# Kernel tuning notes

Hardware: AMD Instinct MI355X
Metric: run time of the kernel (lower is better)

Reference implementation:

```python
import jax, jax.numpy as jnp
import numpy as np

TIMES = 16
SPIKE_THRESHOLD = 1.0
RESET_VALUE = 0.0


def setup_inputs() -> dict:
    key = jax.random.key(0)
    # dim 0 = TIMES * per-step batch (512); feature dim 8192
    inputs = jax.random.normal(key, (TIMES * 512, 8192), dtype=jnp.float32)
    return {"inputs": inputs}


def reference(inputs):
    # torch: inputs.split(shape[0] // times) -> TIMES chunks of [B, D]
    T = TIMES
    B = inputs.shape[0] // T
    xs = inputs.reshape(T, B, inputs.shape[1])  # [T, B, D]

    def step(V, I):
        V = V + I
        # V[V.abs() > thr] = reset_value
        V = jnp.where(jnp.abs(V) > SPIKE_THRESHOLD, jnp.float32(RESET_VALUE), V)
        return V, V

    V0 = jnp.zeros_like(xs[0])
    _, outs = jax.lax.scan(step, V0, xs)  # outs: [T, B, D]
    # torch.vstack(outputs) -> [T*B, D]
    return outs.reshape(inputs.shape)
```

## Files before the change

kernel.cpp:

```cpp
#include <hip/hip_runtime.h>


constexpr int TIMES = 16;
constexpr long long STEP_F4 = (512LL * 8192LL) / 4;

__global__ __launch_bounds__(256) void SpikeLayer_88553635709313_kernel(
    const float4* __restrict__ in, float4* __restrict__ out) {
    long long idx = (long long)blockIdx.x * blockDim.x + threadIdx.x;
    float4 V = make_float4(0.f, 0.f, 0.f, 0.f);
    long long p = idx;
#pragma unroll
    for (int t = 0; t < TIMES; ++t) {
        float4 I = in[p];
        V.x += I.x; V.y += I.y; V.z += I.z; V.w += I.w;
        V.x = (fabsf(V.x) > 1.0f) ? 0.0f : V.x;
        V.y = (fabsf(V.y) > 1.0f) ? 0.0f : V.y;
        V.z = (fabsf(V.z) > 1.0f) ? 0.0f : V.z;
        V.w = (fabsf(V.w) > 1.0f) ? 0.0f : V.w;
        out[p] = V;
        p += STEP_F4;
    }
}

extern "C" void kernel_launch(void* const* d_in, const int* in_sizes, int n_in,
                              void* d_out, int out_size, void* d_ws, size_t ws_size,
                              hipStream_t stream) {
    const float4* in = (const float4*)d_in[0];
    float4* out = (float4*)d_out;
    const int threads = 256;
    const int blocks = (int)(STEP_F4 / threads);
    SpikeLayer_88553635709313_kernel<<<blocks, threads, 0, stream>>>(in, out);
}
```

Baseline: 454.9 us.

## Process two columns per thread with software prefetch and nontemporal stores

Each thread now handles two float4 elements, one from each half of the per-step slab, which halves the grid. The next timestep's input is prefetched before the current step is computed, to raise memory-level parallelism. Outputs are written with nontemporal stores to reduce cache pollution. The risks are lower occupancy from halving the grid and extra register pressure.

```diff
diff --git a/kernel.cpp b/kernel.cpp
--- a/kernel.cpp
+++ b/kernel.cpp
@@ -1,33 +1,57 @@
 #include <hip/hip_runtime.h>
 
 
+typedef float f32x4 __attribute__((ext_vector_type(4)));
+
 constexpr int TIMES = 16;
 constexpr long long STEP_F4 = (512LL * 8192LL) / 4;
+constexpr long long HALF_F4 = STEP_F4 / 2;
+
+__device__ __forceinline__ f32x4 step_reset(f32x4 V, f32x4 I) {
+    V += I;
+    V.x = (fabsf(V.x) > 1.0f) ? 0.0f : V.x;
+    V.y = (fabsf(V.y) > 1.0f) ? 0.0f : V.y;
+    V.z = (fabsf(V.z) > 1.0f) ? 0.0f : V.z;
+    V.w = (fabsf(V.w) > 1.0f) ? 0.0f : V.w;
+    return V;
+}
 
 __global__ __launch_bounds__(256) void SpikeLayer_88553635709313_kernel(
-    const float4* __restrict__ in, float4* __restrict__ out) {
+    const f32x4* __restrict__ in, f32x4* __restrict__ out) {
     long long idx = (long long)blockIdx.x * blockDim.x + threadIdx.x;
-    float4 V = make_float4(0.f, 0.f, 0.f, 0.f);
-    long long p = idx;
+    long long pa = idx;
+    long long pb = idx + HALF_F4;
+
+    f32x4 Va = (f32x4)0.0f;
+    f32x4 Vb = (f32x4)0.0f;
+
+    f32x4 Ia = in[pa];
+    f32x4 Ib = in[pb];
+
 #pragma unroll
     for (int t = 0; t < TIMES; ++t) {
-        float4 I = in[p];
-        V.x += I.x; V.y += I.y; V.z += I.z; V.w += I.w;
-        V.x = (fabsf(V.x) > 1.0f) ? 0.0f : V.x;
-        V.y = (fabsf(V.y) > 1.0f) ? 0.0f : V.y;
-        V.z = (fabsf(V.z) > 1.0f) ? 0.0f : V.z;
-        V.w = (fabsf(V.w) > 1.0f) ? 0.0f : V.w;
-        out[p] = V;
-        p += STEP_F4;
+        f32x4 Na = Ia, Nb = Ib;
+        if (t < TIMES - 1) {
+            Na = in[pa + STEP_F4];
+            Nb = in[pb + STEP_F4];
+        }
+        Va = step_reset(Va, Ia);
+        Vb = step_reset(Vb, Ib);
+        __builtin_nontemporal_store(Va, &out[pa]);
+        __builtin_nontemporal_store(Vb, &out[pb]);
+        pa += STEP_F4;
+        pb += STEP_F4;
+        Ia = Na;
+        Ib = Nb;
     }
 }
 
 extern "C" void kernel_launch(void* const* d_in, const int* in_sizes, int n_in,
                               void* d_out, int out_size, void* d_ws, size_t ws_size,
                               hipStream_t stream) {
-    const float4* in = (const float4*)d_in[0];
-    float4* out = (float4*)d_out;
+    const f32x4* in = (const f32x4*)d_in[0];
+    f32x4* out = (f32x4*)d_out;
     const int threads = 256;
-    const int blocks = (int)(STEP_F4 / threads);
+    const int blocks = (int)(HALF_F4 / threads);
     SpikeLayer_88553635709313_kernel<<<blocks, threads, 0, stream>>>(in, out);
 }
```

After: 474.4 us. 1.04x slower.
